# Kernel tuning notes

Measured on AMD Instinct MI355X. Metric: run time of the kernel, lower is better.

The kernel has to match this reference:

```python
import jax, jax.numpy as jnp
import numpy as np

B, C, H, W = 8, 64, 256, 512
BOUNDARY = 64          # init arg: boundary
DIRECTION = 'lr'       # init arg: direction


def setup_inputs() -> dict:
    key = jax.random.key(0)
    k1, k2 = jax.random.split(key)
    disp = jax.random.uniform(k1, (B, 1, H, W), dtype=jnp.float32)
    target_feature_map = jax.random.normal(k2, (B, C, H, W), dtype=jnp.float32)
    return {"disp": disp, "target_feature_map": target_feature_map}


def _grid_sample_bilinear_zeros(img, gx, gy):
    """F.grid_sample(img, grid) with mode='bilinear', padding_mode='zeros',
    align_corners=False (torch default). img: (b,c,h,w); gx,gy: (b,h,w) in [-1,1]."""
    b, c, h, w = img.shape
    # un-normalize (align_corners=False convention)
    ix = ((gx + 1.0) * w - 1.0) * 0.5
    iy = ((gy + 1.0) * h - 1.0) * 0.5
    x0 = jnp.floor(ix)
    y0 = jnp.floor(iy)
    fx = ix - x0
    fy = iy - y0

    def corner(xi, yi, wgt):
        valid = (xi >= 0) & (xi <= w - 1) & (yi >= 0) & (yi <= h - 1)
        xc = jnp.clip(xi, 0, w - 1).astype(jnp.int32)
        yc = jnp.clip(yi, 0, h - 1).astype(jnp.int32)
        # per-sample gather: (c,h,w) from index maps (h,w)
        g = jax.vmap(lambda im, yy, xx: im[:, yy, xx])(img, yc, xc)  # (b,c,h,w)
        return g * (wgt * valid.astype(img.dtype))[:, None, :, :]

    out = (corner(x0,       y0,       (1 - fx) * (1 - fy))
           + corner(x0 + 1, y0,       fx * (1 - fy))
           + corner(x0,     y0 + 1,   (1 - fx) * fy)
           + corner(x0 + 1, y0 + 1,   fx * fy))
    return out


def reference(disp, target_feature_map):
    b, c, h, w = target_feature_map.shape
    X = jnp.arange(w, dtype=jnp.float32)[None, None, :]   # (1,1,w)
    Y = jnp.arange(h, dtype=jnp.float32)[None, :, None]   # (1,h,1)
    shiftx = (w - 1) / 2.0
    shifty = (h - 1) / 2.0

    if DIRECTION == 'lr':
        mask1d = jnp.arange(w) < (w - BOUNDARY)
        Xs = X + disp[:, 0]                                # (b,h,w)
    else:  # 'rl'
        mask1d = jnp.arange(w) > BOUNDARY
        Xs = X - disp[:, 0]

    gx = (Xs - shiftx) / shiftx                            # (b,h,w)
    gy = jnp.broadcast_to((Y - shifty) / shifty, (b, h, w))

    warped = _grid_sample_bilinear_zeros(target_feature_map, gx, gy)
    mask = jnp.broadcast_to(mask1d[None, None, None, :], (b, c, h, w))
    return warped, mask
```

## Files before the change

kernel.cpp:

```cpp
#include <hip/hip_runtime.h>

#define BB   8
#define CC   64
#define HH   256
#define WW   512
#define BND  64

typedef float f32x4 __attribute__((ext_vector_type(4)));

__global__ __launch_bounds__(256) void warp_feature_kernel(
    const float* __restrict__ disp,
    const float* __restrict__ tgt,
    float* __restrict__ warped,
    float* __restrict__ maskout)
{
    __shared__ float rows[4][WW];

    const int nwg   = BB * CC * (HH / 2);
    const int chunk = nwg / 8;
    const int bid0  = blockIdx.x;
    const int bid   = (bid0 % 8) * chunk + (bid0 / 8);

    const int yq    = bid & (HH / 2 - 1);
    const int ybase = yq * 2;
    const int bc    = bid >> 7;
    const int b     = bc >> 6;
    const int t     = threadIdx.x;

    const float shifty = 127.5f;
    float fyr[2]; int y0cr[2], y1cr[2]; float vy0r[2], vy1r[2];
#pragma unroll
    for (int r = 0; r < 2; ++r) {
        const float yy  = (float)(ybase + r);
        const float gy  = (yy - shifty) / shifty;
        const float iy  = ((gy + 1.0f) * (float)HH - 1.0f) * 0.5f;
        const float y0f = floorf(iy);
        fyr[r]  = iy - y0f;
        const int y0 = (int)y0f;
        const int y1 = y0 + 1;
        vy0r[r] = (y0 >= 0 && y0 <= HH - 1) ? 1.0f : 0.0f;
        vy1r[r] = (y1 >= 0 && y1 <= HH - 1) ? 1.0f : 0.0f;
        y0cr[r] = min(max(y0, 0), HH - 1);
        y1cr[r] = min(max(y1, 0), HH - 1);
    }

    const float* img = tgt + (size_t)bc * (HH * WW);

    const int u7  = t >> 7;
    const int pos = (t & 127) * 4;
    {
        const int ysel0 = u7 ? y1cr[0] : y0cr[0];
        const int ysel1 = u7 ? y1cr[1] : y0cr[1];
        const f32x4 v0 = *reinterpret_cast<const f32x4*>(img + (size_t)ysel0 * WW + pos);
        const f32x4 v1 = *reinterpret_cast<const f32x4*>(img + (size_t)ysel1 * WW + pos);
        *reinterpret_cast<f32x4*>(&rows[u7][pos])     = v0;
        *reinterpret_cast<f32x4*>(&rows[2 + u7][pos]) = v1;
    }
    __syncthreads();

    const int  half = u7;
    const int  y    = ybase + half;
    const float fy  = half ? fyr[1] : fyr[0];
    const float vy0 = half ? vy0r[1] : vy0r[0];
    const float vy1 = half ? vy1r[1] : vy1r[0];
    const float oneMfy = 1.0f - fy;
    const float* rowlo = &rows[half * 2][0];
    const float* rowhi = &rows[half * 2 + 1][0];

    const int xpx = (t & 127) * 4;
    const f32x4 dv = *reinterpret_cast<const f32x4*>(
        disp + ((size_t)b * HH + y) * WW + xpx);

    const float shiftx = 255.5f;

    f32x4 res;
#pragma unroll
    for (int k = 0; k < 4; ++k) {
        const float X   = (float)(xpx + k);
        const float Xs  = X + dv[k];
        const float gx  = (Xs - shiftx) / shiftx;
        const float ix  = ((gx + 1.0f) * (float)WW - 1.0f) * 0.5f;
        const float x0f = floorf(ix);
        const float fx  = ix - x0f;
        const int   x0  = (int)x0f;
        const int   x1  = x0 + 1;
        const float vx0 = (x0 >= 0 && x0 <= WW - 1) ? 1.0f : 0.0f;
        const float vx1 = (x1 >= 0 && x1 <= WW - 1) ? 1.0f : 0.0f;
        const int   x0c = min(max(x0, 0), WW - 1);
        const int   x1c = min(max(x1, 0), WW - 1);

        const float w00 = (1.0f - fx) * oneMfy * vx0 * vy0;
        const float w10 = fx          * oneMfy * vx1 * vy0;
        const float w01 = (1.0f - fx) * fy     * vx0 * vy1;
        const float w11 = fx          * fy     * vx1 * vy1;

        float v = rowlo[x0c] * w00;
        v = fmaf(rowlo[x1c], w10, v);
        v = fmaf(rowhi[x0c], w01, v);
        v = fmaf(rowhi[x1c], w11, v);
        res[k] = v;
    }

    const size_t obase = ((size_t)bc * HH + y) * WW + xpx;
    __builtin_nontemporal_store(res, reinterpret_cast<f32x4*>(warped + obase));

    const float mval = (xpx < (WW - BND)) ? 1.0f : 0.0f;
    f32x4 mv = { mval, mval, mval, mval };
    __builtin_nontemporal_store(mv, reinterpret_cast<f32x4*>(maskout + obase));
}

extern "C" void kernel_launch(void* const* d_in, const int* in_sizes, int n_in,
                              void* d_out, int out_size, void* d_ws, size_t ws_size,
                              hipStream_t stream) {
    const float* disp = (const float*)d_in[0];
    const float* tgt  = (const float*)d_in[1];
    float* warped  = (float*)d_out;
    float* maskout = (float*)d_out + (size_t)BB * CC * HH * WW;

    const int grid = BB * CC * (HH / 2);
    hipLaunchKernelGGL(warp_feature_kernel, dim3(grid), dim3(256), 0, stream,
                       disp, tgt, warped, maskout);
}
```

Baseline: 127.0 us.

## Hoist disp load, simplify coordinate math, use regular stores

The displacement load now happens before the shared-memory staging and barrier, so its latency overlaps with the row loads. The x-coordinate mapping collapses into a single fma, and the bilinear weights are factored into separable horizontal and vertical terms, which cuts ALU work. The output stores go from nontemporal to regular stores. The reassociated float math may differ slightly from the reference in rounding and floor edge cases.

New measurement: 149.6 us. 1.18x slower.

```diff
diff --git a/kernel.cpp b/kernel.cpp
--- a/kernel.cpp
+++ b/kernel.cpp
@@ -27,6 +27,13 @@
     const int b     = bc >> 6;
     const int t     = threadIdx.x;
 
+    const int u7  = t >> 7;
+    const int xpx = (t & 127) * 4;
+    const int y   = ybase + u7;
+
+    const f32x4 dv = *reinterpret_cast<const f32x4*>(
+        disp + ((size_t)b * HH + y) * WW + xpx);
+
     const float shifty = 127.5f;
     float fyr[2]; int y0cr[2], y1cr[2]; float vy0r[2], vy1r[2];
 #pragma unroll
@@ -46,9 +53,8 @@
 
     const float* img = tgt + (size_t)bc * (HH * WW);
 
-    const int u7  = t >> 7;
-    const int pos = (t & 127) * 4;
     {
+        const int pos   = (t & 127) * 4;
         const int ysel0 = u7 ? y1cr[0] : y0cr[0];
         const int ysel1 = u7 ? y1cr[1] : y0cr[1];
         const f32x4 v0 = *reinterpret_cast<const f32x4*>(img + (size_t)ysel0 * WW + pos);
@@ -58,28 +64,21 @@
     }
     __syncthreads();
 
-    const int  half = u7;
-    const int  y    = ybase + half;
-    const float fy  = half ? fyr[1] : fyr[0];
-    const float vy0 = half ? vy0r[1] : vy0r[0];
-    const float vy1 = half ? vy1r[1] : vy1r[0];
-    const float oneMfy = 1.0f - fy;
-    const float* rowlo = &rows[half * 2][0];
-    const float* rowhi = &rows[half * 2 + 1][0];
+    const float fy  = u7 ? fyr[1] : fyr[0];
+    const float vy0 = u7 ? vy0r[1] : vy0r[0];
+    const float vy1 = u7 ? vy1r[1] : vy1r[0];
+    const float cy0 = (1.0f - fy) * vy0;
+    const float cy1 = fy * vy1;
+    const float* rowlo = &rows[u7 * 2][0];
+    const float* rowhi = &rows[u7 * 2 + 1][0];
 
-    const int xpx = (t & 127) * 4;
-    const f32x4 dv = *reinterpret_cast<const f32x4*>(
-        disp + ((size_t)b * HH + y) * WW + xpx);
-
-    const float shiftx = 255.5f;
+    const float IXA = 256.0f / 255.5f;
 
     f32x4 res;
 #pragma unroll
     for (int k = 0; k < 4; ++k) {
-        const float X   = (float)(xpx + k);
-        const float Xs  = X + dv[k];
-        const float gx  = (Xs - shiftx) / shiftx;
-        const float ix  = ((gx + 1.0f) * (float)WW - 1.0f) * 0.5f;
+        const float Xs  = (float)(xpx + k) + dv[k];
+        const float ix  = fmaf(Xs, IXA, -0.5f);
         const float x0f = floorf(ix);
         const float fx  = ix - x0f;
         const int   x0  = (int)x0f;
@@ -89,24 +88,20 @@
         const int   x0c = min(max(x0, 0), WW - 1);
         const int   x1c = min(max(x1, 0), WW - 1);
 
-        const float w00 = (1.0f - fx) * oneMfy * vx0 * vy0;
-        const float w10 = fx          * oneMfy * vx1 * vy0;
-        const float w01 = (1.0f - fx) * fy     * vx0 * vy1;
-        const float w11 = fx          * fy     * vx1 * vy1;
+        const float a0 = (1.0f - fx) * vx0;
+        const float a1 = fx * vx1;
 
-        float v = rowlo[x0c] * w00;
-        v = fmaf(rowlo[x1c], w10, v);
-        v = fmaf(rowhi[x0c], w01, v);
-        v = fmaf(rowhi[x1c], w11, v);
-        res[k] = v;
+        const float h0 = fmaf(rowlo[x1c], a1, rowlo[x0c] * a0);
+        const float h1 = fmaf(rowhi[x1c], a1, rowhi[x0c] * a0);
+        res[k] = fmaf(h1, cy1, h0 * cy0);
     }
 
     const size_t obase = ((size_t)bc * HH + y) * WW + xpx;
-    __builtin_nontemporal_store(res, reinterpret_cast<f32x4*>(warped + obase));
+    *reinterpret_cast<f32x4*>(warped + obase) = res;
 
     const float mval = (xpx < (WW - BND)) ? 1.0f : 0.0f;
     f32x4 mv = { mval, mval, mval, mval };
-    __builtin_nontemporal_store(mv, reinterpret_cast<f32x4*>(maskout + obase));
+    *reinterpret_cast<f32x4*>(maskout + obase) = mv;
 }
 
 extern "C" void kernel_launch(void* const* d_in, const int* in_sizes, int n_in,
```
